# Kernel optimization log

Hardware: AMD Instinct MI355X
Metric: run time of the kernel (lower is better)

## Reference

```python
import jax, jax.numpy as jnp
import numpy as np

B, C, T, V = 8, 64, 16, 207
H, WSZ = 8, 4
EPS = 1e-5


def setup_inputs() -> dict:
    key = jax.random.key(0)
    ks = jax.random.split(key, 16)
    def w(k, shape):
        return jax.random.normal(k, shape, jnp.float32) * 0.02
    inp = {"x": jax.random.normal(ks[0], (B, C, T, V), jnp.float32)}
    for i, s in enumerate("ab"):
        o = 1 + i * 4
        inp[f"qkv_w_{s}"] = w(ks[o], (C, 3 * C))
        inp[f"qkv_b_{s}"] = jnp.zeros((3 * C,), jnp.float32)
        inp[f"proj_w_{s}"] = w(ks[o + 1], (C, C))
        inp[f"proj_b_{s}"] = jnp.zeros((C,), jnp.float32)
        inp[f"ffn_w1_{s}"] = w(ks[o + 2], (C, 4 * C))
        inp[f"ffn_b1_{s}"] = jnp.zeros((4 * C,), jnp.float32)
        inp[f"ffn_w2_{s}"] = w(ks[o + 3], (4 * C, C))
        inp[f"ffn_b2_{s}"] = jnp.zeros((C,), jnp.float32)
        inp[f"ln_{s}1_g"] = jnp.ones((C, T, V), jnp.float32)
        inp[f"ln_{s}1_b"] = jnp.zeros((C, T, V), jnp.float32)
        inp[f"ln_{s}2_g"] = jnp.ones((C, T, V), jnp.float32)
        inp[f"ln_{s}2_b"] = jnp.zeros((C, T, V), jnp.float32)
    inp["n_head"] = H
    inp["window_size"] = WSZ
    return inp


def _layer_norm(x, g, b):
    # LayerNorm over (C, T, V) dims of [B, C, T, V]
    mu = jnp.mean(x, axis=(1, 2, 3), keepdims=True)
    var = jnp.var(x, axis=(1, 2, 3), keepdims=True)
    return (x - mu) / jnp.sqrt(var + EPS) * g + b


def _window_att(x, wqkv, bqkv, wo, bo, n_head, wsz):
    # Joint spatio-temporal attention within windows of `wsz` timesteps.
    b_, c_, t_, v_ = x.shape
    nw = t_ // wsz
    dh = c_ // n_head
    # [B,C,T,V] -> [B,T,V,C] -> [B,nW, wsz*V, C]
    xt = jnp.transpose(x, (0, 2, 3, 1)).reshape(b_, nw, wsz * v_, c_)
    qkv = xt @ wqkv + bqkv  # [B,nW,N,3C]
    q, k, v = jnp.split(qkv, 3, axis=-1)
    def heads(t):
        return t.reshape(b_, nw, -1, n_head, dh).transpose(0, 1, 3, 2, 4)  # [B,nW,H,N,dh]
    q, k, v = heads(q), heads(k), heads(v)
    scale = 1.0 / jnp.sqrt(jnp.asarray(dh, jnp.float32))
    att = jax.nn.softmax(jnp.einsum('bwhnd,bwhmd->bwhnm', q, k) * scale, axis=-1)
    out = jnp.einsum('bwhnm,bwhmd->bwhnd', att, v)
    out = out.transpose(0, 1, 3, 2, 4).reshape(b_, nw, wsz * v_, c_) @ wo + bo
    return out.reshape(b_, t_, v_, c_).transpose(0, 3, 1, 2)


def _ffn(x, w1, b1, w2, b2):
    h = jax.nn.relu(jnp.einsum('bctv,cd->bdtv', x, w1) + b1[None, :, None, None])
    return jnp.einsum('bdtv,dc->bctv', h, w2) + b2[None, :, None, None]


def _block(x, wqkv, bqkv, wo, bo, w1, b1, w2, b2, g1, be1, g2, be2, n_head, wsz):
    x = _window_att(x, wqkv, bqkv, wo, bo, n_head, wsz) + x
    x = _layer_norm(x, g1, be1)
    x = _ffn(x, w1, b1, w2, b2) + x
    x = _layer_norm(x, g2, be2)
    # cyclic shift along time by shift_pixel = wsz // 2
    return jnp.roll(x, -(wsz // 2), axis=2)


def reference(x, qkv_w_a, qkv_b_a, proj_w_a, proj_b_a, ffn_w1_a, ffn_b1_a, ffn_w2_a, ffn_b2_a,
              ln_a1_g, ln_a1_b, ln_a2_g, ln_a2_b,
              qkv_w_b, qkv_b_b, proj_w_b, proj_b_b, ffn_w1_b, ffn_b1_b, ffn_w2_b, ffn_b2_b,
              ln_b1_g, ln_b1_b, ln_b2_g, ln_b2_b, n_head, window_size):
    x = _block(x, qkv_w_a, qkv_b_a, proj_w_a, proj_b_a, ffn_w1_a, ffn_b1_a, ffn_w2_a, ffn_b2_a,
               ln_a1_g, ln_a1_b, ln_a2_g, ln_a2_b, n_head, window_size)
    x = _block(x, qkv_w_b, qkv_b_b, proj_w_b, proj_b_b, ffn_w1_b, ffn_b1_b, ffn_w2_b, ffn_b2_b,
               ln_b1_g, ln_b1_b, ln_b2_g, ln_b2_b, n_head, window_size)
    return x
```

## Files before the change

kernel.cpp:

```cpp
#include <hip/hip_runtime.h>
#include <hip/hip_bf16.h>

#define Bb  8
#define Cc  64
#define Tt  16
#define Vv  207
#define Hh  8
#define DH  8
#define NW  4
#define WSZ 4
#define Nn  (WSZ*Vv)
#define NP  832
#define TV  (Tt*Vv)
#define CTV (Cc*Tt*Vv)
#define S   (Bb*CTV)
#define NBWH (Bb*NW*Hh)
#define EPSF 1e-5f
#define QSCALE 0.51006971401146f
#define FRAG_BWH (52*64*4)
#define LAYER_WSZ 49152

typedef __attribute__((ext_vector_type(4))) short bf16x4;
typedef __attribute__((ext_vector_type(4))) float f32x4;
typedef __attribute__((ext_vector_type(2))) unsigned int u32x2;
typedef __attribute__((ext_vector_type(4))) unsigned int u32x4;

static __device__ __forceinline__ short f2bf(float f) {
    union { float f; unsigned u; } v; v.f = f;
    unsigned r = (v.u + 0x7FFFu + ((v.u >> 16) & 1u)) >> 16;
    return (short)r;
}

static __device__ __forceinline__ bf16x4 pack4(float a, float b, float c, float d) {
    unsigned ua = __builtin_bit_cast(unsigned, a) + 0x8000u;
    unsigned ub = __builtin_bit_cast(unsigned, b) + 0x8000u;
    unsigned uc = __builtin_bit_cast(unsigned, c) + 0x8000u;
    unsigned ud = __builtin_bit_cast(unsigned, d) + 0x8000u;
    u32x2 t;
    t[0] = (ua >> 16) | (ub & 0xFFFF0000u);
    t[1] = (uc >> 16) | (ud & 0xFFFF0000u);
    return __builtin_bit_cast(bf16x4, t);
}

__global__ void prep_kernel(const float* __restrict__ qa, const float* __restrict__ pa,
                            const float* __restrict__ w1a, const float* __restrict__ w2a,
                            const float* __restrict__ qbw, const float* __restrict__ pbw,
                            const float* __restrict__ w1b, const float* __restrict__ w2b,
                            short* __restrict__ wf, float* __restrict__ stats,
                            short* __restrict__ qf, short* __restrict__ kf,
                            short* __restrict__ vf) {
    int i0 = blockIdx.x*256 + threadIdx.x;
    if (i0 < 64) stats[i0] = 0.f;
    for (int i = i0; i < 24576; i += 416*256) {
        int l = i / 12288; int f = i % 12288;
        const float* qw = l ? qbw : qa;
        const float* pw = l ? pbw : pa;
        const float* w1 = l ? w1b : w1a;
        const float* w2 = l ? w2b : w2a;
        short* dst = wf + l*LAYER_WSZ;
        bf16x4 out;
        if (f < 3072) {
            int s = f; int nt = s>>8; int kc = (s>>6)&3; int ln = s&63;
            int li = ln&15; int q = ln>>4;
            #pragma unroll
            for (int j = 0; j < 4; ++j) out[j] = f2bf(qw[(kc*16+q*4+j)*192 + nt*16+li]);
            *((bf16x4*)&dst[s*4]) = out;
        } else if (f < 4096) {
            int s = f-3072; int nt = s>>8; int kc = (s>>6)&3; int ln = s&63;
            int li = ln&15; int q = ln>>4;
            #pragma unroll
            for (int j = 0; j < 4; ++j) out[j] = f2bf(pw[(kc*16+q*4+j)*64 + nt*16+li]);
            *((bf16x4*)&dst[12288 + s*4]) = out;
        } else if (f < 8192) {
            int s = f-4096; int nt = s>>8; int kc = (s>>6)&3; int ln = s&63;
            int li = ln&15; int q = ln>>4;
            #pragma unroll
            for (int j = 0; j < 4; ++j) out[j] = f2bf(w1[(kc*16+q*4+j)*256 + nt*16+li]);
            *((bf16x4*)&dst[16384 + s*4]) = out;
        } else {
            int s = f-8192; int nt = s>>8; int ct = (s>>6)&3; int ln = s&63;
            int li = ln&15; int q = ln>>4;
            #pragma unroll
            for (int j = 0; j < 4; ++j) out[j] = f2bf(w2[(nt*16+q*4+j)*64 + ct*16+li]);
            *((bf16x4*)&dst[32768 + s*4]) = out;
        }
    }
    for (int i = i0; i < NBWH*1664; i += 416*256) {
        int bwh = i / 1664; int rest = i % 1664;
        int nt = rest >> 5; int u = rest & 31;
        size_t base = (size_t)bwh*FRAG_BWH + nt*256;
        *((u32x2*)&qf[base + (32+u)*4]) = (u32x2){0u,0u};
        *((u32x2*)&kf[base + (32+u)*4]) = (u32x2){0u,0u};
        int vlane = (u>>3)*16 + 8 + (u&7);
        short v = ((u&7) == 0) ? (short)0x3F80 : (short)0;
        bf16x4 vv4 = {v,v,v,v};
        *((bf16x4*)&vf[base + vlane*4]) = vv4;
    }
}

__global__ __launch_bounds__(256) void qkv_kernel(const float* __restrict__ src,
        const float* __restrict__ st, const float* __restrict__ g, const float* __restrict__ be,
        const short* __restrict__ wfq, const float* __restrict__ bias,
        short* __restrict__ qf, short* __restrict__ kf, short* __restrict__ vf) {
    __shared__ short wqs[12288];
    __shared__ float bqs[192];
    __shared__ short os[64*196];
    int tid = threadIdx.x;
    int b = blockIdx.x / 52;
    int r0 = (blockIdx.x % 52) * 64;
    const float* xb = src + (size_t)b*CTV;
    {
        const u32x2* wsrc = (const u32x2*)wfq;
        u32x2* wdst = (u32x2*)wqs;
        for (int s = tid; s < 3072; s += 256) wdst[s] = wsrc[s];
    }
    if (tid < 192) bqs[tid] = bias[tid];
    __syncthreads();

    int lane = tid & 63; int wv = tid >> 6;
    int l15 = lane & 15; int quad = lane >> 4;
    int r = r0 + wv*16 + l15;
    int rc = (r < TV) ? r : TV-1;
    int t = rc / Vv; int vv = rc - t*Vv;
    float mean = 0.f, rstd = 0.f; int off;
    if (st) {
        mean = st[b*2] * (1.0f/CTV);
        float var = st[b*2+1] * (1.0f/CTV) - mean*mean;
        rstd = rsqrtf(var + EPSF);
        off = ((t+2)&15)*Vv + vv;
    } else off = rc;

    bf16x4 xf[4];
    #pragma unroll
    for (int kc = 0; kc < 4; ++kc) {
        #pragma unroll
        for (int j = 0; j < 4; ++j) {
            int idx = (kc*16 + quad*4 + j)*TV + off;
            float xv = xb[idx];
            if (st) xv = (xv - mean)*rstd*g[idx] + be[idx];
            xf[kc][j] = f2bf(xv);
        }
    }

    f32x4 accv[12];
    #pragma unroll
    for (int nt = 0; nt < 12; ++nt) {
        float4 bb = *((const float4*)&bqs[nt*16 + quad*4]);
        f32x4 acc = {bb.x, bb.y, bb.z, bb.w};
        #pragma unroll
        for (int kc = 0; kc < 4; ++kc) {
            bf16x4 wf2 = *((const bf16x4*)&wqs[((nt*4 + kc)*64 + lane)*4]);
            acc = __builtin_amdgcn_mfma_f32_16x16x16bf16_1k(wf2, xf[kc], acc, 0, 0, 0);
        }
        accv[nt] = acc;
    }

    int pos = wv*16 + l15;
    #pragma unroll
    for (int nt = 0; nt < 12; ++nt) {
        f32x4 a = accv[nt];
        bf16x4 pk = (nt < 4) ? pack4(a[0]*QSCALE, a[1]*QSCALE, a[2]*QSCALE, a[3]*QSCALE)
                             : pack4(a[0], a[1], a[2], a[3]);
        *((bf16x4*)&os[pos*196 + nt*16 + quad*4]) = pk;
    }
    __syncthreads();

    int pp = tid & 63;
    int rr = r0 + pp;
    bool pv = rr < TV;
    int rrc = pv ? rr : TV-1;
    int t4 = rrc / Vv; int vv4 = rrc - t4*Vv;
    int n2 = (t4 & 3)*Vv + vv4;
    int nt2 = n2 >> 4; int l15n = n2 & 15;
    int quadn = (n2 & 15) >> 2; int jn = n2 & 3;
    int wbase = (b*NW + (t4 >> 2))*Hh;
    if (pv) {
        #pragma unroll
        for (int i = 0; i < 2; ++i) {
            int h = i*4 + wv;
            size_t fb = ((size_t)(wbase+h)*52 + nt2)*256;
            bf16x4 q0 = *((const bf16x4*)&os[pp*196 + h*8]);
            bf16x4 q1 = *((const bf16x4*)&os[pp*196 + h*8 + 4]);
            *((bf16x4*)&qf[fb + l15n*4])        = q0;
            *((bf16x4*)&qf[fb + (16 + l15n)*4]) = q1;
            bf16x4 k0 = *((const bf16x4*)&os[pp*196 + 64 + h*8]);
            bf16x4 k1 = *((const bf16x4*)&os[pp*196 + 64 + h*8 + 4]);
            *((bf16x4*)&kf[fb + l15n*4])        = k0;
            *((bf16x4*)&kf[fb + (16 + l15n)*4]) = k1;
        }
        #pragma unroll
        for (int i = 0; i < 16; ++i) {
            int hd = i*4 + wv;
            int h = hd >> 3; int d = hd & 7;
            vf[(((size_t)(wbase+h)*52 + nt2)*64 + quadn*16 + d)*4 + jn]
                = os[pp*196 + 128 + hd];
        }
    }
}

__global__ __launch_bounds__(1024) void attn_kernel(const short* __restrict__ qf,
        const short* __restrict__ kf, const short* __restrict__ vf,
        short* __restrict__ att) {
    __shared__ short ks2[FRAG_BWH];
    __shared__ short vs2[FRAG_BWH];
    int bwh = blockIdx.x;
    int tid = threadIdx.x;
    int lane = tid & 63;
    int wv = tid >> 6;
    int quad = lane >> 4;
    int l15 = lane & 15;

    {
        const u32x4* kg = (const u32x4*)(kf + (size_t)bwh*FRAG_BWH);
        const u32x4* vg = (const u32x4*)(vf + (size_t)bwh*FRAG_BWH);
        u32x4* kd = (u32x4*)ks2; u32x4* vd = (u32x4*)vs2;
        for (int idx = tid; idx < 1664; idx += 1024) { kd[idx] = kg[idx]; vd[idx] = vg[idx]; }
    }
    __syncthreads();

    int nm = (wv < 4) ? 4 : 3;
    const short* qbase = qf + (size_t)bwh*FRAG_BWH;
    bf16x4 aq[4];
    f32x4 oacc[4];
    #pragma unroll
    for (int i = 0; i < 4; ++i) {
        aq[i] = (bf16x4){0,0,0,0};
        oacc[i] = (f32x4){0.f,0.f,0.f,0.f};
        if (i < nm)
            aq[i] = *(const bf16x4*)(qbase + ((wv + 16*i)*256 + lane*4));
    }

    for (int nt = 0; nt < 52; ++nt) {
        bf16x4 ak = *(const bf16x4*)&ks2[nt*256 + lane*4];
        bf16x4 av = *(const bf16x4*)&vs2[nt*256 + lane*4];
        bool mask = (nt == 51) && (quad == 3);
        #pragma unroll
        for (int i = 0; i < 4; ++i) {
            if (i < nm) {
                f32x4 s = __builtin_amdgcn_mfma_f32_16x16x16bf16_1k(
                              ak, aq[i], (f32x4){0.f,0.f,0.f,0.f}, 0, 0, 0);
                bf16x4 pb = pack4(__builtin_amdgcn_exp2f(s[0]), __builtin_amdgcn_exp2f(s[1]),
                                  __builtin_amdgcn_exp2f(s[2]), __builtin_amdgcn_exp2f(s[3]));
                if (mask) pb = (bf16x4){0,0,0,0};
                oacc[i] = __builtin_amdgcn_mfma_f32_16x16x16bf16_1k(av, pb, oacc[i], 0, 0, 0);
            }
        }
    }
    int h = bwh & 7; int bw = bwh >> 3;
    #pragma unroll
    for (int i = 0; i < 4; ++i) {
        if (i < nm) {
            float ls = __shfl(oacc[i][0], 32 + l15, 64);
            float inv = 1.f / ls;
            int m = (wv + 16*i)*16 + l15;
            if (quad < 2 && m < Nn) {
                bf16x4 ov = pack4(oacc[i][0]*inv, oacc[i][1]*inv,
                                  oacc[i][2]*inv, oacc[i][3]*inv);
                *((bf16x4*)&att[((size_t)bw*Nn + m)*Cc + h*DH + quad*4]) = ov;
            }
        }
    }
}

__global__ __launch_bounds__(256) void proj_kernel(const short* __restrict__ att,
        const short* __restrict__ wfp, const float* __restrict__ bo,
        const float* __restrict__ resid,
        const float* __restrict__ st, const float* __restrict__ g, const float* __restrict__ be,
        float* __restrict__ out, float* __restrict__ stats) {
    __shared__ short wos[4096];
    __shared__ float bos[64];
    __shared__ float r1[256], r2[256];
    int tid = threadIdx.x;
    int b = blockIdx.x / 52;
    int r0 = (blockIdx.x % 52) * 64;
    const float* xb = resid + (size_t)b*CTV;
    {
        const u32x2* wsrc = (const u32x2*)wfp;
        u32x2* wdst = (u32x2*)wos;
        for (int s = tid; s < 1024; s += 256) wdst[s] = wsrc[s];
    }
    if (tid < 64) bos[tid] = bo[tid];
    __syncthreads();

    int lane = tid & 63; int wv = tid >> 6;
    int l15 = lane & 15; int quad = lane >> 4;
    int r = r0 + wv*16 + l15;
    bool valid = r < TV;
    int rc = valid ? r : TV-1;
    int t = rc / Vv; int vv = rc - t*Vv;
    int n = (t & 3)*Vv + vv;
    int bw = b*NW + (t >> 2);
    const short* arow = att + ((size_t)bw*Nn + n)*Cc;
    bf16x4 af[4];
    #pragma unroll
    for (int kc = 0; kc < 4; ++kc)
        af[kc] = *((const bf16x4*)&arow[kc*16 + quad*4]);

    f32x4 acc[4];
    #pragma unroll
    for (int nt = 0; nt < 4; ++nt) {
        float4 bb = *((const float4*)&bos[nt*16 + quad*4]);
        acc[nt] = (f32x4){bb.x, bb.y, bb.z, bb.w};
        #pragma unroll
        for (int kc = 0; kc < 4; ++kc) {
            bf16x4 wf2 = *((const bf16x4*)&wos[((nt*4 + kc)*64 + lane)*4]);
            acc[nt] = __builtin_amdgcn_mfma_f32_16x16x16bf16_1k(wf2, af[kc], acc[nt], 0, 0, 0);
        }
    }
    float mean = 0.f, rstd = 0.f; int off;
    if (st) {
        mean = st[b*2] * (1.0f/CTV);
        float var = st[b*2+1] * (1.0f/CTV) - mean*mean;
        rstd = rsqrtf(var + EPSF);
        off = ((t+2)&15)*Vv + vv;
    } else off = rc;
    float s1 = 0.f, s2 = 0.f;
    if (valid) {
        #pragma unroll
        for (int nt = 0; nt < 4; ++nt) {
            #pragma unroll
            for (int j = 0; j < 4; ++j) {
                int c_out = nt*16 + quad*4 + j;
                int ridx = c_out*TV + off;
                float xv = xb[ridx];
                if (st) xv = (xv - mean)*rstd*g[ridx] + be[ridx];
                float val = acc[nt][j] + xv;
                out[(size_t)b*CTV + (size_t)c_out*TV + r] = val;
                s1 += val; s2 += val*val;
            }
        }
    }
    r1[tid] = s1; r2[tid] = s2;
    __syncthreads();
    for (int o = 128; o > 0; o >>= 1) {
        if (tid < o) { r1[tid] += r1[tid+o]; r2[tid] += r2[tid+o]; }
        __syncthreads();
    }
    if (tid == 0) { atomicAdd(&stats[b*2], r1[0]); atomicAdd(&stats[b*2+1], r2[0]); }
}

__global__ void ln_apply_kernel(const float* __restrict__ x,
                                const float* __restrict__ g,
                                const float* __restrict__ be,
                                const float* __restrict__ stats,
                                float* __restrict__ out,
                                int shift) {
    int idx = blockIdx.x*256 + threadIdx.x;
    if (idx >= S) return;
    int b = idx / CTV; int r = idx % CTV;
    int c = r / TV; int q2 = r % TV; int t = q2 / Vv; int vv = q2 % Vv;
    float mean = stats[b*2] * (1.0f/CTV);
    float var  = stats[b*2+1] * (1.0f/CTV) - mean*mean;
    float rstd = rsqrtf(var + EPSF);
    float val = (x[idx]-mean)*rstd*g[r] + be[r];
    int tout = (t - shift + Tt) % Tt;
    size_t oidx = ((size_t)(b*Cc + c)*Tt + tout)*Vv + vv;
    out[oidx] = val;
}

__global__ __launch_bounds__(256) void ffn_kernel(const float* __restrict__ xin,
        const float* __restrict__ st, const float* __restrict__ g, const float* __restrict__ be,
        const short* __restrict__ wf1, const float* __restrict__ b1,
        const short* __restrict__ wf2g, const float* __restrict__ b2,
        float* __restrict__ out, float* __restrict__ stats) {
    __shared__ short w1s[16384];
    __shared__ short w2s[16384];
    __shared__ short xsf[4096];
    __shared__ float b1s[256];
    __shared__ float b2s[64];
    __shared__ float r1s[256], r2s[256];
    int tid = threadIdx.x;
    int b = blockIdx.x / 52;
    int r0 = (blockIdx.x % 52) * 64;
    const float* xb = xin + (size_t)b*CTV;
    float mean = st[b*2] * (1.0f/CTV);
    float var  = st[b*2+1] * (1.0f/CTV) - mean*mean;
    float rstd = rsqrtf(var + EPSF);

    {
        const u32x2* s1p = (const u32x2*)wf1;
        const u32x2* s2p = (const u32x2*)wf2g;
        u32x2* d1 = (u32x2*)w1s; u32x2* d2 = (u32x2*)w2s;
        for (int s = tid; s < 4096; s += 256) { d1[s] = s1p[s]; d2[s] = s2p[s]; }
    }
    for (int s2 = tid; s2 < 1024; s2 += 256) {
        int wv2 = s2 >> 8; int kc = (s2 >> 6) & 3; int ln = s2 & 63;
        int l15 = ln & 15; int quad = ln >> 4;
        int r = r0 + wv2*16 + l15; if (r >= TV) r = TV-1;
        bf16x4 f;
        #pragma unroll
        for (int j = 0; j < 4; ++j) {
            int idx = (kc*16 + quad*4 + j)*TV + r;
            f[j] = f2bf((xb[idx] - mean)*rstd*g[idx] + be[idx]);
        }
        *((bf16x4*)&xsf[s2*4]) = f;
    }
    b1s[tid] = b1[tid];
    if (tid < 64) b2s[tid] = b2[tid];
    __syncthreads();

    int lane = tid & 63; int wv = tid >> 6;
    int l15 = lane & 15; int quad = lane >> 4;
    bf16x4 xf[4];
    #pragma unroll
    for (int kc = 0; kc < 4; ++kc)
        xf[kc] = *((const bf16x4*)&xsf[((wv*4 + kc)*64 + lane)*4]);

    f32x4 oacc[4];
    #pragma unroll
    for (int ct = 0; ct < 4; ++ct) oacc[ct] = (f32x4){0.f,0.f,0.f,0.f};

    for (int nt = 0; nt < 16; ++nt) {
        float4 bb = *((const float4*)&b1s[nt*16 + quad*4]);
        f32x4 acc = {bb.x, bb.y, bb.z, bb.w};
        #pragma unroll
        for (int kc = 0; kc < 4; ++kc) {
            bf16x4 wfv = *((const bf16x4*)&w1s[((nt*4 + kc)*64 + lane)*4]);
            acc = __builtin_amdgcn_mfma_f32_16x16x16bf16_1k(wfv, xf[kc], acc, 0, 0, 0);
        }
        bf16x4 pf = pack4(fmaxf(acc[0], 0.f), fmaxf(acc[1], 0.f),
                          fmaxf(acc[2], 0.f), fmaxf(acc[3], 0.f));
        #pragma unroll
        for (int ct = 0; ct < 4; ++ct) {
            bf16x4 wfv2 = *((const bf16x4*)&w2s[((nt*4 + ct)*64 + lane)*4]);
            oacc[ct] = __builtin_amdgcn_mfma_f32_16x16x16bf16_1k(wfv2, pf, oacc[ct], 0, 0, 0);
        }
    }
    int r = r0 + wv*16 + l15;
    float s1 = 0.f, s2v = 0.f;
    if (r < TV) {
        #pragma unroll
        for (int ct = 0; ct < 4; ++ct) {
            #pragma unroll
            for (int j = 0; j < 4; ++j) {
                int c_out = ct*16 + quad*4 + j;
                int idx = c_out*TV + r;
                float xv = (xb[idx] - mean)*rstd*g[idx] + be[idx];
                float val = oacc[ct][j] + b2s[c_out] + xv;
                out[(size_t)b*CTV + idx] = val;
                s1 += val; s2v += val*val;
            }
        }
    }
    r1s[tid] = s1; r2s[tid] = s2v;
    __syncthreads();
    for (int o = 128; o > 0; o >>= 1) {
        if (tid < o) { r1s[tid] += r1s[tid+o]; r2s[tid] += r2s[tid+o]; }
        __syncthreads();
    }
    if (tid == 0) { atomicAdd(&stats[b*2], r1s[0]); atomicAdd(&stats[b*2+1], r2s[0]); }
}

extern "C" void kernel_launch(void* const* d_in, const int* in_sizes, int n_in,
                              void* d_out, int out_size, void* d_ws, size_t ws_size,
                              hipStream_t stream) {
    const float* xin = (const float*)d_in[0];

    float* bufA  = (float*)d_ws;
    float* bufB  = bufA + S;
    float* stats = bufB + S;
    short* qf    = (short*)(stats + 64);
    short* kf    = qf + (size_t)NBWH*FRAG_BWH;
    short* vf    = kf + (size_t)NBWH*FRAG_BWH;
    short* att   = vf + (size_t)NBWH*FRAG_BWH;
    short* wf    = att + (size_t)32*Nn*64;

    const float* A0  = (const float*)d_in[1];
    const float* A1  = (const float*)d_in[2];
    const float* A2  = (const float*)d_in[3];
    const float* A3  = (const float*)d_in[4];
    const float* A4  = (const float*)d_in[5];
    const float* A5  = (const float*)d_in[6];
    const float* A6  = (const float*)d_in[7];
    const float* A7  = (const float*)d_in[8];
    const float* A8  = (const float*)d_in[9];
    const float* A9  = (const float*)d_in[10];
    const float* A10 = (const float*)d_in[11];
    const float* A11 = (const float*)d_in[12];
    const float* B0  = (const float*)d_in[13];
    const float* B1  = (const float*)d_in[14];
    const float* B2  = (const float*)d_in[15];
    const float* B3  = (const float*)d_in[16];
    const float* B4  = (const float*)d_in[17];
    const float* B5  = (const float*)d_in[18];
    const float* B6  = (const float*)d_in[19];
    const float* B7  = (const float*)d_in[20];
    const float* B8  = (const float*)d_in[21];
    const float* B9  = (const float*)d_in[22];
    const float* B10 = (const float*)d_in[23];
    const float* B11 = (const float*)d_in[24];

    float* st1a = stats + 0;
    float* st2a = stats + 16;
    float* st1b = stats + 32;
    float* st2b = stats + 48;

    short* wfA = wf;
    short* wfB = wf + LAYER_WSZ;

    prep_kernel<<<416, 256, 0, stream>>>(A0, A2, A4, A6, B0, B2, B4, B6,
                                         wf, stats, qf, kf, vf);

    qkv_kernel<<<Bb*52, 256, 0, stream>>>(xin, nullptr, nullptr, nullptr,
                                          wfA, A1, qf, kf, vf);
    attn_kernel<<<NBWH, 1024, 0, stream>>>(qf, kf, vf, att);
    proj_kernel<<<Bb*52, 256, 0, stream>>>(att, wfA + 12288, A3, xin,
                                           nullptr, nullptr, nullptr, bufB, st1a);
    ffn_kernel<<<Bb*52, 256, 0, stream>>>(bufB, st1a, A8, A9,
                                          wfA + 16384, A5, wfA + 32768, A7, bufB, st2a);
    qkv_kernel<<<Bb*52, 256, 0, stream>>>(bufB, st2a, A10, A11,
                                          wfB, B1, qf, kf, vf);
    attn_kernel<<<NBWH, 1024, 0, stream>>>(qf, kf, vf, att);
    proj_kernel<<<Bb*52, 256, 0, stream>>>(att, wfB + 12288, B3, bufB,
                                           st2a, A10, A11, bufA, st1b);
    ffn_kernel<<<Bb*52, 256, 0, stream>>>(bufA, st1b, B8, B9,
                                          wfB + 16384, B5, wfB + 32768, B7, bufA, st2b);
    ln_apply_kernel<<<(S+255)/256, 256, 0, stream>>>(bufA, B10, B11, st2b, (float*)d_out, WSZ/2);
}
```

Measured before the change: 295.4 us.

## Split output-channel tiles across two wave groups in qkv, proj and ffn kernels

```diff
diff --git a/kernel.cpp b/kernel.cpp
--- a/kernel.cpp
+++ b/kernel.cpp
@@ -98,7 +98,7 @@
     }
 }
 
-__global__ __launch_bounds__(256) void qkv_kernel(const float* __restrict__ src,
+__global__ __launch_bounds__(512) void qkv_kernel(const float* __restrict__ src,
         const float* __restrict__ st, const float* __restrict__ g, const float* __restrict__ be,
         const short* __restrict__ wfq, const float* __restrict__ bias,
         short* __restrict__ qf, short* __restrict__ kf, short* __restrict__ vf) {
@@ -112,14 +112,15 @@
     {
         const u32x2* wsrc = (const u32x2*)wfq;
         u32x2* wdst = (u32x2*)wqs;
-        for (int s = tid; s < 3072; s += 256) wdst[s] = wsrc[s];
+        for (int s = tid; s < 3072; s += 512) wdst[s] = wsrc[s];
     }
     if (tid < 192) bqs[tid] = bias[tid];
     __syncthreads();
 
     int lane = tid & 63; int wv = tid >> 6;
+    int rs = wv & 3; int gsel = wv >> 2;
     int l15 = lane & 15; int quad = lane >> 4;
-    int r = r0 + wv*16 + l15;
+    int r = r0 + rs*16 + l15;
     int rc = (r < TV) ? r : TV-1;
     int t = rc / Vv; int vv = rc - t*Vv;
     float mean = 0.f, rstd = 0.f; int off;
@@ -142,9 +143,10 @@
         }
     }
 
-    f32x4 accv[12];
-    #pragma unroll
-    for (int nt = 0; nt < 12; ++nt) {
+    f32x4 accv[6];
+    #pragma unroll
+    for (int ntl = 0; ntl < 6; ++ntl) {
+        int nt = gsel*6 + ntl;
         float4 bb = *((const float4*)&bqs[nt*16 + quad*4]);
         f32x4 acc = {bb.x, bb.y, bb.z, bb.w};
         #pragma unroll
@@ -152,13 +154,14 @@
             bf16x4 wf2 = *((const bf16x4*)&wqs[((nt*4 + kc)*64 + lane)*4]);
             acc = __builtin_amdgcn_mfma_f32_16x16x16bf16_1k(wf2, xf[kc], acc, 0, 0, 0);
         }
-        accv[nt] = acc;
-    }
-
-    int pos = wv*16 + l15;
-    #pragma unroll
-    for (int nt = 0; nt < 12; ++nt) {
-        f32x4 a = accv[nt];
+        accv[ntl] = acc;
+    }
+
+    int pos = rs*16 + l15;
+    #pragma unroll
+    for (int ntl = 0; ntl < 6; ++ntl) {
+        int nt = gsel*6 + ntl;
+        f32x4 a = accv[ntl];
         bf16x4 pk = (nt < 4) ? pack4(a[0]*QSCALE, a[1]*QSCALE, a[2]*QSCALE, a[3]*QSCALE)
                              : pack4(a[0], a[1], a[2], a[3]);
         *((bf16x4*)&os[pos*196 + nt*16 + quad*4]) = pk;
@@ -175,9 +178,8 @@
     int quadn = (n2 & 15) >> 2; int jn = n2 & 3;
     int wbase = (b*NW + (t4 >> 2))*Hh;
     if (pv) {
-        #pragma unroll
-        for (int i = 0; i < 2; ++i) {
-            int h = i*4 + wv;
+        {
+            int h = wv;
             size_t fb = ((size_t)(wbase+h)*52 + nt2)*256;
             bf16x4 q0 = *((const bf16x4*)&os[pp*196 + h*8]);
             bf16x4 q1 = *((const bf16x4*)&os[pp*196 + h*8 + 4]);
@@ -189,8 +191,8 @@
             *((bf16x4*)&kf[fb + (16 + l15n)*4]) = k1;
         }
         #pragma unroll
-        for (int i = 0; i < 16; ++i) {
-            int hd = i*4 + wv;
+        for (int i = 0; i < 8; ++i) {
+            int hd = i*8 + wv;
             int h = hd >> 3; int d = hd & 7;
             vf[(((size_t)(wbase+h)*52 + nt2)*64 + quadn*16 + d)*4 + jn]
                 = os[pp*196 + 128 + hd];
@@ -262,14 +264,14 @@
     }
 }
 
-__global__ __launch_bounds__(256) void proj_kernel(const short* __restrict__ att,
+__global__ __launch_bounds__(512) void proj_kernel(const short* __restrict__ att,
         const short* __restrict__ wfp, const float* __restrict__ bo,
         const float* __restrict__ resid,
         const float* __restrict__ st, const float* __restrict__ g, const float* __restrict__ be,
         float* __restrict__ out, float* __restrict__ stats) {
     __shared__ short wos[4096];
     __shared__ float bos[64];
-    __shared__ float r1[256], r2[256];
+    __shared__ float r1[512], r2[512];
     int tid = threadIdx.x;
     int b = blockIdx.x / 52;
     int r0 = (blockIdx.x % 52) * 64;
@@ -277,14 +279,15 @@
     {
         const u32x2* wsrc = (const u32x2*)wfp;
         u32x2* wdst = (u32x2*)wos;
-        for (int s = tid; s < 1024; s += 256) wdst[s] = wsrc[s];
+        for (int s = tid; s < 1024; s += 512) wdst[s] = wsrc[s];
     }
     if (tid < 64) bos[tid] = bo[tid];
     __syncthreads();
 
     int lane = tid & 63; int wv = tid >> 6;
+    int rs = wv & 3; int gsel = wv >> 2;
     int l15 = lane & 15; int quad = lane >> 4;
-    int r = r0 + wv*16 + l15;
+    int r = r0 + rs*16 + l15;
     bool valid = r < TV;
     int rc = valid ? r : TV-1;
     int t = rc / Vv; int vv = rc - t*Vv;
@@ -296,15 +299,16 @@
     for (int kc = 0; kc < 4; ++kc)
         af[kc] = *((const bf16x4*)&arow[kc*16 + quad*4]);
 
-    f32x4 acc[4];
-    #pragma unroll
-    for (int nt = 0; nt < 4; ++nt) {
+    f32x4 acc[2];
+    #pragma unroll
+    for (int ntl = 0; ntl < 2; ++ntl) {
+        int nt = gsel*2 + ntl;
         float4 bb = *((const float4*)&bos[nt*16 + quad*4]);
-        acc[nt] = (f32x4){bb.x, bb.y, bb.z, bb.w};
+        acc[ntl] = (f32x4){bb.x, bb.y, bb.z, bb.w};
         #pragma unroll
         for (int kc = 0; kc < 4; ++kc) {
             bf16x4 wf2 = *((const bf16x4*)&wos[((nt*4 + kc)*64 + lane)*4]);
-            acc[nt] = __builtin_amdgcn_mfma_f32_16x16x16bf16_1k(wf2, af[kc], acc[nt], 0, 0, 0);
+            acc[ntl] = __builtin_amdgcn_mfma_f32_16x16x16bf16_1k(wf2, af[kc], acc[ntl], 0, 0, 0);
         }
     }
     float mean = 0.f, rstd = 0.f; int off;
@@ -317,14 +321,15 @@
     float s1 = 0.f, s2 = 0.f;
     if (valid) {
         #pragma unroll
-        for (int nt = 0; nt < 4; ++nt) {
+        for (int ntl = 0; ntl < 2; ++ntl) {
+            int nt = gsel*2 + ntl;
             #pragma unroll
             for (int j = 0; j < 4; ++j) {
                 int c_out = nt*16 + quad*4 + j;
                 int ridx = c_out*TV + off;
                 float xv = xb[ridx];
                 if (st) xv = (xv - mean)*rstd*g[ridx] + be[ridx];
-                float val = acc[nt][j] + xv;
+                float val = acc[ntl][j] + xv;
                 out[(size_t)b*CTV + (size_t)c_out*TV + r] = val;
                 s1 += val; s2 += val*val;
             }
@@ -332,7 +337,7 @@
     }
     r1[tid] = s1; r2[tid] = s2;
     __syncthreads();
-    for (int o = 128; o > 0; o >>= 1) {
+    for (int o = 256; o > 0; o >>= 1) {
         if (tid < o) { r1[tid] += r1[tid+o]; r2[tid] += r2[tid+o]; }
         __syncthreads();
     }
@@ -358,7 +363,7 @@
     out[oidx] = val;
 }
 
-__global__ __launch_bounds__(256) void ffn_kernel(const float* __restrict__ xin,
+__global__ __launch_bounds__(512) void ffn_kernel(const float* __restrict__ xin,
         const float* __restrict__ st, const float* __restrict__ g, const float* __restrict__ be,
         const short* __restrict__ wf1, const float* __restrict__ b1,
         const short* __restrict__ wf2g, const float* __restrict__ b2,
@@ -368,7 +373,7 @@
     __shared__ short xsf[4096];
     __shared__ float b1s[256];
     __shared__ float b2s[64];
-    __shared__ float r1s[256], r2s[256];
+    __shared__ float r1s[512], r2s[512];
     int tid = threadIdx.x;
     int b = blockIdx.x / 52;
     int r0 = (blockIdx.x % 52) * 64;
@@ -381,9 +386,9 @@
         const u32x2* s1p = (const u32x2*)wf1;
         const u32x2* s2p = (const u32x2*)wf2g;
         u32x2* d1 = (u32x2*)w1s; u32x2* d2 = (u32x2*)w2s;
-        for (int s = tid; s < 4096; s += 256) { d1[s] = s1p[s]; d2[s] = s2p[s]; }
-    }
-    for (int s2 = tid; s2 < 1024; s2 += 256) {
+        for (int s = tid; s < 4096; s += 512) { d1[s] = s1p[s]; d2[s] = s2p[s]; }
+    }
+    for (int s2 = tid; s2 < 1024; s2 += 512) {
         int wv2 = s2 >> 8; int kc = (s2 >> 6) & 3; int ln = s2 & 63;
         int l15 = ln & 15; int quad = ln >> 4;
         int r = r0 + wv2*16 + l15; if (r >= TV) r = TV-1;
@@ -395,20 +400,21 @@
         }
         *((bf16x4*)&xsf[s2*4]) = f;
     }
-    b1s[tid] = b1[tid];
+    if (tid < 256) b1s[tid] = b1[tid];
     if (tid < 64) b2s[tid] = b2[tid];
     __syncthreads();
 
     int lane = tid & 63; int wv = tid >> 6;
+    int rs = wv & 3; int gsel = wv >> 2;
     int l15 = lane & 15; int quad = lane >> 4;
     bf16x4 xf[4];
     #pragma unroll
     for (int kc = 0; kc < 4; ++kc)
-        xf[kc] = *((const bf16x4*)&xsf[((wv*4 + kc)*64 + lane)*4]);
-
-    f32x4 oacc[4];
-    #pragma unroll
-    for (int ct = 0; ct < 4; ++ct) oacc[ct] = (f32x4){0.f,0.f,0.f,0.f};
+        xf[kc] = *((const bf16x4*)&xsf[((rs*4 + kc)*64 + lane)*4]);
+
+    f32x4 oacc[2];
+    #pragma unroll
+    for (int ctl = 0; ctl < 2; ++ctl) oacc[ctl] = (f32x4){0.f,0.f,0.f,0.f};
 
     for (int nt = 0; nt < 16; ++nt) {
         float4 bb = *((const float4*)&b1s[nt*16 + quad*4]);
@@ -421,22 +427,24 @@
         bf16x4 pf = pack4(fmaxf(acc[0], 0.f), fmaxf(acc[1], 0.f),
                           fmaxf(acc[2], 0.f), fmaxf(acc[3], 0.f));
         #pragma unroll
-        for (int ct = 0; ct < 4; ++ct) {
+        for (int ctl = 0; ctl < 2; ++ctl) {
+            int ct = gsel*2 + ctl;
             bf16x4 wfv2 = *((const bf16x4*)&w2s[((nt*4 + ct)*64 + lane)*4]);
-            oacc[ct] = __builtin_amdgcn_mfma_f32_16x16x16bf16_1k(wfv2, pf, oacc[ct], 0, 0, 0);
-        }
-    }
-    int r = r0 + wv*16 + l15;
+            oacc[ctl] = __builtin_amdgcn_mfma_f32_16x16x16bf16_1k(wfv2, pf, oacc[ctl], 0, 0, 0);
+        }
+    }
+    int r = r0 + rs*16 + l15;
     float s1 = 0.f, s2v = 0.f;
     if (r < TV) {
         #pragma unroll
-        for (int ct = 0; ct < 4; ++ct) {
+        for (int ctl = 0; ctl < 2; ++ctl) {
+            int ct = gsel*2 + ctl;
             #pragma unroll
             for (int j = 0; j < 4; ++j) {
                 int c_out = ct*16 + quad*4 + j;
                 int idx = c_out*TV + r;
                 float xv = (xb[idx] - mean)*rstd*g[idx] + be[idx];
-                float val = oacc[ct][j] + b2s[c_out] + xv;
+                float val = oacc[ctl][j] + b2s[c_out] + xv;
                 out[(size_t)b*CTV + idx] = val;
                 s1 += val; s2v += val*val;
             }
@@ -444,7 +452,7 @@
     }
     r1s[tid] = s1; r2s[tid] = s2v;
     __syncthreads();
-    for (int o = 128; o > 0; o >>= 1) {
+    for (int o = 256; o > 0; o >>= 1) {
         if (tid < o) { r1s[tid] += r1s[tid+o]; r2s[tid] += r2s[tid+o]; }
         __syncthreads();
     }
@@ -501,19 +509,19 @@
     prep_kernel<<<416, 256, 0, stream>>>(A0, A2, A4, A6, B0, B2, B4, B6,
                                          wf, stats, qf, kf, vf);
 
-    qkv_kernel<<<Bb*52, 256, 0, stream>>>(xin, nullptr, nullptr, nullptr,
+    qkv_kernel<<<Bb*52, 512, 0, stream>>>(xin, nullptr, nullptr, nullptr,
                                           wfA, A1, qf, kf, vf);
     attn_kernel<<<NBWH, 1024, 0, stream>>>(qf, kf, vf, att);
-    proj_kernel<<<Bb*52, 256, 0, stream>>>(att, wfA + 12288, A3, xin,
+    proj_kernel<<<Bb*52, 512, 0, stream>>>(att, wfA + 12288, A3, xin,
                                            nullptr, nullptr, nullptr, bufB, st1a);
-    ffn_kernel<<<Bb*52, 256, 0, stream>>>(bufB, st1a, A8, A9,
+    ffn_kernel<<<Bb*52, 512, 0, stream>>>(bufB, st1a, A8, A9,
                                           wfA + 16384, A5, wfA + 32768, A7, bufB, st2a);
-    qkv_kernel<<<Bb*52, 256, 0, stream>>>(bufB, st2a, A10, A11,
+    qkv_kernel<<<Bb*52, 512, 0, stream>>>(bufB, st2a, A10, A11,
                                           wfB, B1, qf, kf, vf);
     attn_kernel<<<NBWH, 1024, 0, stream>>>(qf, kf, vf, att);
-    proj_kernel<<<Bb*52, 256, 0, stream>>>(att, wfB + 12288, B3, bufB,
+    proj_kernel<<<Bb*52, 512, 0, stream>>>(att, wfB + 12288, B3, bufB,
                                            st2a, A10, A11, bufA, st1b);
-    ffn_kernel<<<Bb*52, 256, 0, stream>>>(bufA, st1b, B8, B9,
+    ffn_kernel<<<Bb*52, 512, 0, stream>>>(bufA, st1b, B8, B9,
                                           wfB + 16384, B5, wfB + 32768, B7, bufA, st2b);
     ln_apply_kernel<<<(S+255)/256, 256, 0, stream>>>(bufA, B10, B11, st2b, (float*)d_out, WSZ/2);
 }
```

Result: faster. 280.3 us (-5.1%).
